# Kernel tuning notes

Measured on AMD Instinct MI355X. Metric: run time of the kernel, lower is better.

The kernel has to match this reference:

```python
import jax, jax.numpy as jnp
import numpy as np

NB = 8            # num_blocks
BS = 96           # block_size = hidden_size // num_blocks
HSF = 1           # hidden_size_factor
LAM = 0.01        # sparsity_threshold (softshrink lambda)
FRAC = 1.0        # hard_thresholding_fraction
SCALE = 0.02


def setup_inputs() -> dict:
    key = jax.random.key(0)
    ks = jax.random.split(key, 9)
    B, C, H, W, D = 2, NB * BS, 32, 32, 32
    x = jax.random.normal(ks[0], (B, C, H, W, D), jnp.float32)
    # complex params stored as separate real/imag float arrays (torch.rand on cfloat
    # fills real and imag independently with U[0,1))
    w1r = SCALE * jax.random.uniform(ks[1], (NB, BS, BS * HSF), jnp.float32)
    w1i = SCALE * jax.random.uniform(ks[2], (NB, BS, BS * HSF), jnp.float32)
    w2r = SCALE * jax.random.uniform(ks[3], (NB, BS, BS * HSF), jnp.float32)
    w2i = SCALE * jax.random.uniform(ks[4], (NB, BS, BS * HSF), jnp.float32)
    b1r = SCALE * jax.random.uniform(ks[5], (NB, BS * HSF), jnp.float32)
    b1i = SCALE * jax.random.uniform(ks[6], (NB, BS * HSF), jnp.float32)
    b2r = SCALE * jax.random.uniform(ks[7], (NB, BS), jnp.float32)
    b2i = SCALE * jax.random.uniform(ks[8], (NB, BS), jnp.float32)
    return {"x": x, "w1r": w1r, "w1i": w1i, "w2r": w2r, "w2i": w2i,
            "b1r": b1r, "b1i": b1i, "b2r": b2r, "b2i": b2i}


def _softshrink(v, lam):
    return jnp.sign(v) * jnp.maximum(jnp.abs(v) - lam, 0.0)


def _gelu_c(z):
    # torch GELU applied to view_as_real => separately on real and imag parts
    return jax.nn.gelu(jnp.real(z), approximate=False) + 1j * jax.nn.gelu(jnp.imag(z), approximate=False)


def reference(x, w1r, w1i, w2r, w2i, b1r, b1i, b2r, b2i):
    bias = x
    B, C, H, W, D = x.shape
    w1 = w1r + 1j * w1i
    w2 = w2r + 1j * w2i
    b1 = b1r + 1j * b1i
    b2 = b2r + 1j * b2i

    xf = jnp.fft.rfftn(x.astype(jnp.float32), axes=(-3, -2, -1), norm='ortho')
    Dr = xf.shape[-1]                      # D//2 + 1
    xf = xf.reshape(B, NB, BS, H, W, Dr)

    total_modes = H * W * D // 2 + 1
    kept = min(int(total_modes * FRAC), Dr)  # original slices only the last freq axis
    xk = xf[..., :kept]                      # (B, nb, bs, H, W, kept)

    # block-diagonal complex GEMM 1 + bias, then GELU on real/imag parts
    h1 = jnp.einsum('bnihwd,nio->bnohwd', xk, w1) + b1[None, :, :, None, None, None]
    h1 = _gelu_c(h1)
    # block-diagonal complex GEMM 2 + bias
    h2 = jnp.einsum('bnihwd,nio->bnohwd', h1, w2) + b2[None, :, :, None, None, None]

    # scatter back into full spectrum (zeros beyond kept modes)
    if kept < Dr:
        h2 = jnp.pad(h2, ((0, 0), (0, 0), (0, 0), (0, 0), (0, 0), (0, Dr - kept)))

    # softshrink on real/imag parts
    z = _softshrink(jnp.real(h2), LAM) + 1j * _softshrink(jnp.imag(h2), LAM)
    z = z.reshape(B, C, H, W, Dr)
    out = jnp.fft.irfftn(z, s=(H, W, D), axes=(-3, -2, -1), norm='ortho')
    return out.astype(x.dtype) + bias
```

## Files before the change

kernel.cpp:

```cpp
#include <hip/hip_runtime.h>
#include <math.h>


#define CH    768
#define DR    17
#define PLANE 544
#define NVOL  49152
#define CSTRIDE 17408
#define NTOT  26738688
#define ORTHO 0.0055242717280199026f
#define TWOPI_32 0.19634954084936207f

typedef __bf16 bf16x8 __attribute__((ext_vector_type(8)));
typedef __bf16 bf16x2 __attribute__((ext_vector_type(2)));
typedef float  f32x4  __attribute__((ext_vector_type(4)));

#define MFMA __builtin_amdgcn_mfma_f32_16x16x32_bf16

__device__ __forceinline__ float gelu_f(float v) {
    return 0.5f * v * (1.0f + erff(v * 0.7071067811865475f));
}
__device__ __forceinline__ float sshrink(float v) {
    float a = fabsf(v) - 0.01f;
    return a > 0.f ? copysignf(a, v) : 0.f;
}
__device__ __forceinline__ bf16x8 ld8(const __bf16* p) { return *(const bf16x8*)p; }
__device__ __forceinline__ void split2(float v, __bf16* h, __bf16* l) {
    __bf16 hh = (__bf16)v;
    *h = hh;
    *l = (__bf16)(v - (float)hh);
}

__device__ __align__(16) __bf16 gEf[4][1024];
__device__ __align__(16) __bf16 gEb[4][1024];
__device__ __align__(16) __bf16 gC [4][1024];

__global__ void k0_tables() {
    int idx = blockIdx.x * 256 + threadIdx.x;
    if (idx >= 1024) return;
    int c = idx & 31;
    int r = idx >> 5;
    float ang = TWOPI_32 * (float)((r * c) & 31);
    float s, co; sincosf(ang, &s, &co);
    __bf16 h, l;
    split2(co, &h, &l);  gEf[0][idx] = h; gEf[1][idx] = l;
                         gEb[0][idx] = h; gEb[1][idx] = l;
    split2(-s, &h, &l);  gEf[2][idx] = h; gEf[3][idx] = l;
    split2(s, &h, &l);   gEb[2][idx] = h; gEb[3][idx] = l;
    float cf = (c == 0 || c == 16) ? 1.f : (c < DR ? 2.f : 0.f);
    split2(cf * co, &h, &l); gC[0][idx] = h; gC[1][idx] = l;
    split2(-cf * s, &h, &l); gC[2][idx] = h; gC[3][idx] = l;
}

__device__ __align__(16) __bf16 gW1r[73728], gW1i[73728], gW2r[73728], gW2i[73728];

__global__ void k0w(const float* __restrict__ w1r, const float* __restrict__ w1i,
                    const float* __restrict__ w2r, const float* __restrict__ w2i) {
    int idx = blockIdx.x * 256 + threadIdx.x;
    if (idx >= 73728) return;
    int i = idx % 96, no = idx / 96;
    int o = no % 96, n = no / 96;
    int src = n * 9216 + i * 96 + o;
    gW1r[idx] = (__bf16)w1r[src];
    gW1i[idx] = (__bf16)w1i[src];
    gW2r[idx] = (__bf16)w2r[src];
    gW2i[idx] = (__bf16)w2i[src];
}

__global__ __launch_bounds__(256) void k1_fwd_dw(const float* __restrict__ x,
                                                 bf16x2* __restrict__ A) {
    __shared__ __align__(16) __bf16 sArh[2][32][40], sArl[2][32][40], sAih[2][32][40], sAil[2][32][40];
    const int t = threadIdx.x;
    const int wave = t >> 6, lane = t & 63, row = lane & 15, quad = lane >> 4;
    const int m0 = (wave >> 1) * 16, n0 = (wave & 1) * 16;
    const size_t pb = (size_t)blockIdx.x * 2048;

    bf16x8 xh[2], xl[2];
    #pragma unroll
    for (int pl = 0; pl < 2; pl++) {
        const float* xp = x + pb + pl * 1024 + (size_t)(m0 + row) * 32 + quad * 8;
        f32x4 x0 = *(const f32x4*)xp;
        f32x4 x1 = *(const f32x4*)(xp + 4);
        #pragma unroll
        for (int j = 0; j < 4; j++) { __bf16 h = (__bf16)x0[j]; xh[pl][j] = h; xl[pl][j] = (__bf16)(x0[j] - (float)h); }
        #pragma unroll
        for (int j = 0; j < 4; j++) { __bf16 h = (__bf16)x1[j]; xh[pl][4+j] = h; xl[pl][4+j] = (__bf16)(x1[j] - (float)h); }
    }

    {
        const int ed = (n0 + row) * 32 + quad * 8;
        bf16x8 erh = *(const bf16x8*)&gEf[0][ed];
        bf16x8 erl = *(const bf16x8*)&gEf[1][ed];
        bf16x8 eih = *(const bf16x8*)&gEf[2][ed];
        bf16x8 eil = *(const bf16x8*)&gEf[3][ed];
        #pragma unroll
        for (int pl = 0; pl < 2; pl++) {
            f32x4 ar = {0.f,0.f,0.f,0.f}, ai = {0.f,0.f,0.f,0.f};
            ar = MFMA(xh[pl], erh, ar, 0,0,0); ar = MFMA(xh[pl], erl, ar, 0,0,0); ar = MFMA(xl[pl], erh, ar, 0,0,0);
            ai = MFMA(xh[pl], eih, ai, 0,0,0); ai = MFMA(xh[pl], eil, ai, 0,0,0); ai = MFMA(xl[pl], eih, ai, 0,0,0);
            #pragma unroll
            for (int r4 = 0; r4 < 4; r4++) {
                int w = m0 + quad * 4 + r4, kd = n0 + row;
                split2(ar[r4], &sArh[pl][kd][w], &sArl[pl][kd][w]);
                split2(ai[r4], &sAih[pl][kd][w], &sAil[pl][kd][w]);
            }
        }
    }
    __syncthreads();
    {
        const int ew = (m0 + row) * 32 + quad * 8;
        bf16x8 frh = *(const bf16x8*)&gEf[0][ew];
        bf16x8 frl = *(const bf16x8*)&gEf[1][ew];
        bf16x8 fih = *(const bf16x8*)&gEf[2][ew];
        bf16x8 fil = *(const bf16x8*)&gEf[3][ew];
        const int kd = n0 + row;
        #pragma unroll
        for (int pl = 0; pl < 2; pl++) {
            bf16x8 arh = ld8(&sArh[pl][n0 + row][quad * 8]);
            bf16x8 arl = ld8(&sArl[pl][n0 + row][quad * 8]);
            bf16x8 aih = ld8(&sAih[pl][n0 + row][quad * 8]);
            bf16x8 ail = ld8(&sAil[pl][n0 + row][quad * 8]);
            f32x4 rp = {0.f,0.f,0.f,0.f}, rm = {0.f,0.f,0.f,0.f}, im = {0.f,0.f,0.f,0.f};
            rp = MFMA(frh, arh, rp, 0,0,0); rp = MFMA(frh, arl, rp, 0,0,0); rp = MFMA(frl, arh, rp, 0,0,0);
            rm = MFMA(fih, aih, rm, 0,0,0); rm = MFMA(fih, ail, rm, 0,0,0); rm = MFMA(fil, aih, rm, 0,0,0);
            im = MFMA(frh, aih, im, 0,0,0); im = MFMA(frh, ail, im, 0,0,0); im = MFMA(frl, aih, im, 0,0,0);
            im = MFMA(fih, arh, im, 0,0,0); im = MFMA(fih, arl, im, 0,0,0); im = MFMA(fil, arh, im, 0,0,0);
            if (kd < DR) {
                const size_t ab = ((size_t)blockIdx.x * 2 + pl) * PLANE;
                #pragma unroll
                for (int r4 = 0; r4 < 4; r4++) {
                    int kw = m0 + quad * 4 + r4;
                    bf16x2 o;
                    o.x = (__bf16)((rp[r4] - rm[r4]) * ORTHO);
                    o.y = (__bf16)(im[r4] * ORTHO);
                    A[ab + kw * DR + kd] = o;
                }
            }
        }
    }
}

template <bool INV>
__global__ __launch_bounds__(256) void k2_fft_h(bf16x2* __restrict__ A) {
    __shared__ __align__(16) __bf16 sBr[272][40], sBi[272][40];
    const int t = threadIdx.x;
    const int p0g = blockIdx.x * 272;
    const size_t cb = (size_t)blockIdx.y * CSTRIDE;
    for (int idx = t; idx < 8704; idx += 256) {
        int h = idx / 272, p = idx - h * 272;
        bf16x2 v = A[cb + (size_t)h * PLANE + p0g + p];
        sBr[p][h] = v.x;
        sBi[p][h] = v.y;
    }
    __syncthreads();
    const int wave = t >> 6, lane = t & 63, row = lane & 15, quad = lane >> 4;
    const __bf16* Er = gEf[0];
    const __bf16* Ei = INV ? gEb[2] : gEf[2];
    bf16x8 er0 = *(const bf16x8*)&Er[row * 32 + quad * 8];
    bf16x8 ei0 = *(const bf16x8*)&Ei[row * 32 + quad * 8];
    bf16x8 er1 = *(const bf16x8*)&Er[(16 + row) * 32 + quad * 8];
    bf16x8 ei1 = *(const bf16x8*)&Ei[(16 + row) * 32 + quad * 8];
    for (int j = wave; j < 34; j += 4) {
        int mt = j & 1, nt = j >> 1;
        int m0 = mt * 16, n0 = nt * 16;
        bf16x8 ar = mt ? er1 : er0;
        bf16x8 ai = mt ? ei1 : ei0;
        bf16x8 br = ld8(&sBr[n0 + row][quad * 8]);
        bf16x8 bi = ld8(&sBi[n0 + row][quad * 8]);
        f32x4 rp = {0.f,0.f,0.f,0.f}, rm = {0.f,0.f,0.f,0.f}, im = {0.f,0.f,0.f,0.f};
        rp = MFMA(ar, br, rp, 0, 0, 0);
        rm = MFMA(ai, bi, rm, 0, 0, 0);
        im = MFMA(ar, bi, im, 0, 0, 0);
        im = MFMA(ai, br, im, 0, 0, 0);
        int p = p0g + n0 + row;
        #pragma unroll
        for (int r = 0; r < 4; r++) {
            int kh = m0 + quad * 4 + r;
            size_t oidx = cb + (size_t)kh * PLANE + p;
            if (!INV) {
                bf16x2 o;
                o.x = (__bf16)(rp[r] - rm[r]);
                o.y = (__bf16)im[r];
                A[oidx] = o;
            } else {
                __bf16 rh, rl, ih, il;
                split2(rp[r] - rm[r], &rh, &rl);
                split2(im[r], &ih, &il);
                bf16x2 oh; oh.x = rh; oh.y = ih;
                bf16x2 ol; ol.x = rl; ol.y = il;
                A[oidx] = oh;
                A[NTOT + oidx] = ol;
            }
        }
    }
}

__global__ __launch_bounds__(256) void k3_mix(bf16x2* __restrict__ A,
    const float* __restrict__ b1r, const float* __restrict__ b1i,
    const float* __restrict__ b2r, const float* __restrict__ b2i) {
    __shared__ __align__(16) __bf16 sXr[64][104], sXi[64][104];
    const int t = threadIdx.x;
    const int chunk = blockIdx.x, bn = blockIdx.y;
    const int b = bn >> 3, n = bn & 7;
    const size_t base = (size_t)(b * CH + n * 96) * CSTRIDE + chunk * 64;

    for (int idx = t; idx < 6144; idx += 256) {
        int i = idx >> 6, p = idx & 63;
        bf16x2 v = A[base + (size_t)i * CSTRIDE + p];
        sXr[p][i] = v.x;
        sXi[p][i] = v.y;
    }
    __syncthreads();

    const int wave = t >> 6, lane = t & 63, row = lane & 15, quad = lane >> 4;
    const __bf16* W1r = &gW1r[n * 9216];
    const __bf16* W1i = &gW1i[n * 9216];
    const __bf16* W2r = &gW2r[n * 9216];
    const __bf16* W2i = &gW2i[n * 9216];
    float h1s[6][8];

    #pragma unroll
    for (int q = 0; q < 6; q++) {
        int job = wave * 6 + q, mt = job >> 2, nt = job & 3;
        int m0 = mt * 16, p0 = nt * 16;
        f32x4 rp = {0.f,0.f,0.f,0.f}, rm = {0.f,0.f,0.f,0.f}, im = {0.f,0.f,0.f,0.f};
        #pragma unroll
        for (int ks = 0; ks < 3; ks++) {
            int k0 = ks * 32 + quad * 8;
            bf16x8 ar = ld8(&W1r[(m0 + row) * 96 + k0]);
            bf16x8 ai = ld8(&W1i[(m0 + row) * 96 + k0]);
            bf16x8 br = ld8(&sXr[p0 + row][k0]);
            bf16x8 bi = ld8(&sXi[p0 + row][k0]);
            rp = MFMA(ar, br, rp, 0, 0, 0);
            rm = MFMA(ai, bi, rm, 0, 0, 0);
            im = MFMA(ar, bi, im, 0, 0, 0);
            im = MFMA(ai, br, im, 0, 0, 0);
        }
        #pragma unroll
        for (int r = 0; r < 4; r++) {
            int o = m0 + quad * 4 + r;
            float hr = b1r[n * 96 + o] + rp[r] - rm[r];
            float hi = b1i[n * 96 + o] + im[r];
            h1s[q][r]     = gelu_f(hr);
            h1s[q][4 + r] = gelu_f(hi);
        }
    }
    __syncthreads();

    #pragma unroll
    for (int q = 0; q < 6; q++) {
        int job = wave * 6 + q, mt = job >> 2, nt = job & 3;
        int m0 = mt * 16, p0 = nt * 16;
        int p = p0 + row;
        #pragma unroll
        for (int r = 0; r < 4; r++) {
            int o = m0 + quad * 4 + r;
            sXr[p][o] = (__bf16)h1s[q][r];
            sXi[p][o] = (__bf16)h1s[q][4 + r];
        }
    }
    __syncthreads();

    #pragma unroll
    for (int q = 0; q < 6; q++) {
        int job = wave * 6 + q, mt = job >> 2, nt = job & 3;
        int m0 = mt * 16, p0 = nt * 16;
        f32x4 rp = {0.f,0.f,0.f,0.f}, rm = {0.f,0.f,0.f,0.f}, im = {0.f,0.f,0.f,0.f};
        #pragma unroll
        for (int ks = 0; ks < 3; ks++) {
            int k0 = ks * 32 + quad * 8;
            bf16x8 ar = ld8(&W2r[(m0 + row) * 96 + k0]);
            bf16x8 ai = ld8(&W2i[(m0 + row) * 96 + k0]);
            bf16x8 br = ld8(&sXr[p0 + row][k0]);
            bf16x8 bi = ld8(&sXi[p0 + row][k0]);
            rp = MFMA(ar, br, rp, 0, 0, 0);
            rm = MFMA(ai, bi, rm, 0, 0, 0);
            im = MFMA(ar, bi, im, 0, 0, 0);
            im = MFMA(ai, br, im, 0, 0, 0);
        }
        int p = p0 + row;
        #pragma unroll
        for (int r = 0; r < 4; r++) {
            int o = m0 + quad * 4 + r;
            bf16x2 oV;
            oV.x = (__bf16)sshrink(b2r[n * 96 + o] + rp[r] - rm[r]);
            oV.y = (__bf16)sshrink(b2i[n * 96 + o] + im[r]);
            A[base + (size_t)o * CSTRIDE + p] = oV;
        }
    }
}

__global__ __launch_bounds__(256) void k5_inv_wd(const bf16x2* __restrict__ A,
                                                 const float* __restrict__ x,
                                                 float* __restrict__ out) {
    __shared__ __align__(16) __bf16 sZrh[32][40], sZrl[32][40], sZih[32][40], sZil[32][40];
    const int t = threadIdx.x;
    const int wave = t >> 6, lane = t & 63, row = lane & 15, quad = lane >> 4;
    const int m0 = (wave >> 1) * 16, n0 = (wave & 1) * 16;
    const size_t ab = (size_t)blockIdx.x * PLANE;
    const size_t pb = (size_t)blockIdx.x * 1024;
    const int d = n0 + row;

    float xres[4];
    #pragma unroll
    for (int r4 = 0; r4 < 4; r4++)
        xres[r4] = x[pb + (size_t)(m0 + quad * 4 + r4) * 32 + d];

    for (int idx = t; idx < PLANE; idx += 256) {
        int kw = idx / DR, kd = idx - kw * DR;
        bf16x2 h = A[ab + idx];
        bf16x2 l = A[NTOT + ab + idx];
        sZrh[kd][kw] = h.x; sZrl[kd][kw] = l.x;
        sZih[kd][kw] = h.y; sZil[kd][kw] = l.y;
    }
    for (int idx = t; idx < 480; idx += 256) {
        int kd = DR + (idx >> 5), kw = idx & 31;
        sZrh[kd][kw] = (__bf16)0.f; sZrl[kd][kw] = (__bf16)0.f;
        sZih[kd][kw] = (__bf16)0.f; sZil[kd][kw] = (__bf16)0.f;
    }
    __syncthreads();

    const int e1 = (m0 + row) * 32 + quad * 8;
    bf16x8 erh = *(const bf16x8*)&gEb[0][e1];
    bf16x8 erl = *(const bf16x8*)&gEb[1][e1];
    bf16x8 eih = *(const bf16x8*)&gEb[2][e1];
    bf16x8 eil = *(const bf16x8*)&gEb[3][e1];
    bf16x8 zrh = ld8(&sZrh[n0 + row][quad * 8]);
    bf16x8 zrl = ld8(&sZrl[n0 + row][quad * 8]);
    bf16x8 zih = ld8(&sZih[n0 + row][quad * 8]);
    bf16x8 zil = ld8(&sZil[n0 + row][quad * 8]);
    f32x4 rp = {0.f,0.f,0.f,0.f}, rm = {0.f,0.f,0.f,0.f}, im = {0.f,0.f,0.f,0.f};
    rp = MFMA(erh, zrh, rp, 0,0,0); rp = MFMA(erh, zrl, rp, 0,0,0); rp = MFMA(erl, zrh, rp, 0,0,0);
    rm = MFMA(eih, zih, rm, 0,0,0); rm = MFMA(eih, zil, rm, 0,0,0); rm = MFMA(eil, zih, rm, 0,0,0);
    im = MFMA(erh, zih, im, 0,0,0); im = MFMA(erh, zil, im, 0,0,0); im = MFMA(erl, zih, im, 0,0,0);
    im = MFMA(eih, zrh, im, 0,0,0); im = MFMA(eih, zrl, im, 0,0,0); im = MFMA(eil, zrh, im, 0,0,0);
    __syncthreads();
    #pragma unroll
    for (int r4 = 0; r4 < 4; r4++) {
        int w = m0 + quad * 4 + r4, kd = n0 + row;
        split2(rp[r4] - rm[r4], &sZrh[w][kd], &sZrl[w][kd]);
        split2(im[r4],          &sZih[w][kd], &sZil[w][kd]);
    }
    __syncthreads();

    const int c2 = d * 32 + quad * 8;
    bf16x8 crh = *(const bf16x8*)&gC[0][c2];
    bf16x8 crl = *(const bf16x8*)&gC[1][c2];
    bf16x8 cih = *(const bf16x8*)&gC[2][c2];
    bf16x8 cil = *(const bf16x8*)&gC[3][c2];
    bf16x8 grh = ld8(&sZrh[m0 + row][quad * 8]);
    bf16x8 grl = ld8(&sZrl[m0 + row][quad * 8]);
    bf16x8 gih = ld8(&sZih[m0 + row][quad * 8]);
    bf16x8 gil = ld8(&sZil[m0 + row][quad * 8]);
    f32x4 acc = {0.f,0.f,0.f,0.f};
    acc = MFMA(grh, crh, acc, 0,0,0); acc = MFMA(grh, crl, acc, 0,0,0); acc = MFMA(grl, crh, acc, 0,0,0);
    acc = MFMA(gih, cih, acc, 0,0,0); acc = MFMA(gih, cil, acc, 0,0,0); acc = MFMA(gil, cih, acc, 0,0,0);
    #pragma unroll
    for (int r4 = 0; r4 < 4; r4++) {
        int w = m0 + quad * 4 + r4;
        out[pb + (size_t)w * 32 + d] = acc[r4] * ORTHO + xres[r4];
    }
}

extern "C" void kernel_launch(void* const* d_in, const int* in_sizes, int n_in,
                              void* d_out, int out_size, void* d_ws, size_t ws_size,
                              hipStream_t stream) {
    const float* x   = (const float*)d_in[0];
    const float* w1r = (const float*)d_in[1];
    const float* w1i = (const float*)d_in[2];
    const float* w2r = (const float*)d_in[3];
    const float* w2i = (const float*)d_in[4];
    const float* b1r = (const float*)d_in[5];
    const float* b1i = (const float*)d_in[6];
    const float* b2r = (const float*)d_in[7];
    const float* b2i = (const float*)d_in[8];
    float* out = (float*)d_out;
    bf16x2* A = (bf16x2*)d_ws;

    k0_tables<<<4, 256, 0, stream>>>();
    k0w<<<288, 256, 0, stream>>>(w1r, w1i, w2r, w2i);
    k1_fwd_dw<<<NVOL / 2, 256, 0, stream>>>(x, A);
    k2_fft_h<false><<<dim3(2, 1536), 256, 0, stream>>>(A);
    k3_mix<<<dim3(272, 16), 256, 0, stream>>>(A, b1r, b1i, b2r, b2i);
    k2_fft_h<true><<<dim3(2, 1536), 256, 0, stream>>>(A);
    k5_inv_wd<<<NVOL, 256, 0, stream>>>(A, x, out);
}
```

Measured before the change: 847.6 us.

## Process more planes per block and stage mixing weights in shared memory

The forward D/W transform kernel now handles four planes per block instead of two, and the inverse W/D kernel handles two planes per block instead of one. This amortizes the per-block twiddle-table loads and launch overhead over more work. The block-diagonal mixing kernel now copies each block's W1 and then W2 weight slices into shared memory before the MFMA loops, instead of reading them from global memory in every inner iteration. The cost is more shared memory and registers per block, which may reduce occupancy, and fewer blocks in the grid.

```diff
diff --git a/kernel.cpp b/kernel.cpp
--- a/kernel.cpp
+++ b/kernel.cpp
@@ -69,15 +69,15 @@
 
 __global__ __launch_bounds__(256) void k1_fwd_dw(const float* __restrict__ x,
                                                  bf16x2* __restrict__ A) {
-    __shared__ __align__(16) __bf16 sArh[2][32][40], sArl[2][32][40], sAih[2][32][40], sAil[2][32][40];
+    __shared__ __align__(16) __bf16 sArh[4][32][40], sArl[4][32][40], sAih[4][32][40], sAil[4][32][40];
     const int t = threadIdx.x;
     const int wave = t >> 6, lane = t & 63, row = lane & 15, quad = lane >> 4;
     const int m0 = (wave >> 1) * 16, n0 = (wave & 1) * 16;
-    const size_t pb = (size_t)blockIdx.x * 2048;
-
-    bf16x8 xh[2], xl[2];
-    #pragma unroll
-    for (int pl = 0; pl < 2; pl++) {
+    const size_t pb = (size_t)blockIdx.x * 4096;
+
+    bf16x8 xh[4], xl[4];
+    #pragma unroll
+    for (int pl = 0; pl < 4; pl++) {
         const float* xp = x + pb + pl * 1024 + (size_t)(m0 + row) * 32 + quad * 8;
         f32x4 x0 = *(const f32x4*)xp;
         f32x4 x1 = *(const f32x4*)(xp + 4);
@@ -94,7 +94,7 @@
         bf16x8 eih = *(const bf16x8*)&gEf[2][ed];
         bf16x8 eil = *(const bf16x8*)&gEf[3][ed];
         #pragma unroll
-        for (int pl = 0; pl < 2; pl++) {
+        for (int pl = 0; pl < 4; pl++) {
             f32x4 ar = {0.f,0.f,0.f,0.f}, ai = {0.f,0.f,0.f,0.f};
             ar = MFMA(xh[pl], erh, ar, 0,0,0); ar = MFMA(xh[pl], erl, ar, 0,0,0); ar = MFMA(xl[pl], erh, ar, 0,0,0);
             ai = MFMA(xh[pl], eih, ai, 0,0,0); ai = MFMA(xh[pl], eil, ai, 0,0,0); ai = MFMA(xl[pl], eih, ai, 0,0,0);
@@ -115,7 +115,7 @@
         bf16x8 fil = *(const bf16x8*)&gEf[3][ew];
         const int kd = n0 + row;
         #pragma unroll
-        for (int pl = 0; pl < 2; pl++) {
+        for (int pl = 0; pl < 4; pl++) {
             bf16x8 arh = ld8(&sArh[pl][n0 + row][quad * 8]);
             bf16x8 arl = ld8(&sArl[pl][n0 + row][quad * 8]);
             bf16x8 aih = ld8(&sAih[pl][n0 + row][quad * 8]);
@@ -126,7 +126,7 @@
             im = MFMA(frh, aih, im, 0,0,0); im = MFMA(frh, ail, im, 0,0,0); im = MFMA(frl, aih, im, 0,0,0);
             im = MFMA(fih, arh, im, 0,0,0); im = MFMA(fih, arl, im, 0,0,0); im = MFMA(fil, arh, im, 0,0,0);
             if (kd < DR) {
-                const size_t ab = ((size_t)blockIdx.x * 2 + pl) * PLANE;
+                const size_t ab = ((size_t)blockIdx.x * 4 + pl) * PLANE;
                 #pragma unroll
                 for (int r4 = 0; r4 < 4; r4++) {
                     int kw = m0 + quad * 4 + r4;
@@ -198,12 +198,18 @@
 __global__ __launch_bounds__(256) void k3_mix(bf16x2* __restrict__ A,
     const float* __restrict__ b1r, const float* __restrict__ b1i,
     const float* __restrict__ b2r, const float* __restrict__ b2i) {
+    __shared__ __align__(16) __bf16 sWr[96][104], sWi[96][104];
     __shared__ __align__(16) __bf16 sXr[64][104], sXi[64][104];
     const int t = threadIdx.x;
     const int chunk = blockIdx.x, bn = blockIdx.y;
     const int b = bn >> 3, n = bn & 7;
     const size_t base = (size_t)(b * CH + n * 96) * CSTRIDE + chunk * 64;
 
+    for (int j = t; j < 1152; j += 256) {
+        int rw = j / 12, off = j - rw * 12;
+        *(bf16x8*)&sWr[rw][off * 8] = *(const bf16x8*)&gW1r[n * 9216 + j * 8];
+        *(bf16x8*)&sWi[rw][off * 8] = *(const bf16x8*)&gW1i[n * 9216 + j * 8];
+    }
     for (int idx = t; idx < 6144; idx += 256) {
         int i = idx >> 6, p = idx & 63;
         bf16x2 v = A[base + (size_t)i * CSTRIDE + p];
@@ -213,10 +219,6 @@
     __syncthreads();
 
     const int wave = t >> 6, lane = t & 63, row = lane & 15, quad = lane >> 4;
-    const __bf16* W1r = &gW1r[n * 9216];
-    const __bf16* W1i = &gW1i[n * 9216];
-    const __bf16* W2r = &gW2r[n * 9216];
-    const __bf16* W2i = &gW2i[n * 9216];
     float h1s[6][8];
 
     #pragma unroll
@@ -227,8 +229,8 @@
         #pragma unroll
         for (int ks = 0; ks < 3; ks++) {
             int k0 = ks * 32 + quad * 8;
-            bf16x8 ar = ld8(&W1r[(m0 + row) * 96 + k0]);
-            bf16x8 ai = ld8(&W1i[(m0 + row) * 96 + k0]);
+            bf16x8 ar = ld8(&sWr[m0 + row][k0]);
+            bf16x8 ai = ld8(&sWi[m0 + row][k0]);
             bf16x8 br = ld8(&sXr[p0 + row][k0]);
             bf16x8 bi = ld8(&sXi[p0 + row][k0]);
             rp = MFMA(ar, br, rp, 0, 0, 0);
@@ -259,6 +261,11 @@
             sXi[p][o] = (__bf16)h1s[q][4 + r];
         }
     }
+    for (int j = t; j < 1152; j += 256) {
+        int rw = j / 12, off = j - rw * 12;
+        *(bf16x8*)&sWr[rw][off * 8] = *(const bf16x8*)&gW2r[n * 9216 + j * 8];
+        *(bf16x8*)&sWi[rw][off * 8] = *(const bf16x8*)&gW2i[n * 9216 + j * 8];
+    }
     __syncthreads();
 
     #pragma unroll
@@ -269,8 +276,8 @@
         #pragma unroll
         for (int ks = 0; ks < 3; ks++) {
             int k0 = ks * 32 + quad * 8;
-            bf16x8 ar = ld8(&W2r[(m0 + row) * 96 + k0]);
-            bf16x8 ai = ld8(&W2i[(m0 + row) * 96 + k0]);
+            bf16x8 ar = ld8(&sWr[m0 + row][k0]);
+            bf16x8 ai = ld8(&sWi[m0 + row][k0]);
             bf16x8 br = ld8(&sXr[p0 + row][k0]);
             bf16x8 bi = ld8(&sXi[p0 + row][k0]);
             rp = MFMA(ar, br, rp, 0, 0, 0);
@@ -293,30 +300,34 @@
 __global__ __launch_bounds__(256) void k5_inv_wd(const bf16x2* __restrict__ A,
                                                  const float* __restrict__ x,
                                                  float* __restrict__ out) {
-    __shared__ __align__(16) __bf16 sZrh[32][40], sZrl[32][40], sZih[32][40], sZil[32][40];
+    __shared__ __align__(16) __bf16 sZrh[2][32][40], sZrl[2][32][40], sZih[2][32][40], sZil[2][32][40];
     const int t = threadIdx.x;
     const int wave = t >> 6, lane = t & 63, row = lane & 15, quad = lane >> 4;
     const int m0 = (wave >> 1) * 16, n0 = (wave & 1) * 16;
-    const size_t ab = (size_t)blockIdx.x * PLANE;
-    const size_t pb = (size_t)blockIdx.x * 1024;
+    const size_t ab = (size_t)blockIdx.x * (2 * PLANE);
+    const size_t pb = (size_t)blockIdx.x * 2048;
     const int d = n0 + row;
 
-    float xres[4];
-    #pragma unroll
-    for (int r4 = 0; r4 < 4; r4++)
-        xres[r4] = x[pb + (size_t)(m0 + quad * 4 + r4) * 32 + d];
-
-    for (int idx = t; idx < PLANE; idx += 256) {
-        int kw = idx / DR, kd = idx - kw * DR;
+    float xres[2][4];
+    #pragma unroll
+    for (int pl = 0; pl < 2; pl++)
+        #pragma unroll
+        for (int r4 = 0; r4 < 4; r4++)
+            xres[pl][r4] = x[pb + pl * 1024 + (size_t)(m0 + quad * 4 + r4) * 32 + d];
+
+    for (int idx = t; idx < 2 * PLANE; idx += 256) {
+        int pl = idx / PLANE, li = idx - pl * PLANE;
+        int kw = li / DR, kd = li - kw * DR;
         bf16x2 h = A[ab + idx];
         bf16x2 l = A[NTOT + ab + idx];
-        sZrh[kd][kw] = h.x; sZrl[kd][kw] = l.x;
-        sZih[kd][kw] = h.y; sZil[kd][kw] = l.y;
-    }
-    for (int idx = t; idx < 480; idx += 256) {
-        int kd = DR + (idx >> 5), kw = idx & 31;
-        sZrh[kd][kw] = (__bf16)0.f; sZrl[kd][kw] = (__bf16)0.f;
-        sZih[kd][kw] = (__bf16)0.f; sZil[kd][kw] = (__bf16)0.f;
+        sZrh[pl][kd][kw] = h.x; sZrl[pl][kd][kw] = l.x;
+        sZih[pl][kd][kw] = h.y; sZil[pl][kd][kw] = l.y;
+    }
+    for (int idx = t; idx < 960; idx += 256) {
+        int pl = idx / 480, r = idx - pl * 480;
+        int kd = DR + (r >> 5), kw = r & 31;
+        sZrh[pl][kd][kw] = (__bf16)0.f; sZrl[pl][kd][kw] = (__bf16)0.f;
+        sZih[pl][kd][kw] = (__bf16)0.f; sZil[pl][kd][kw] = (__bf16)0.f;
     }
     __syncthreads();
 
@@ -325,21 +336,30 @@
     bf16x8 erl = *(const bf16x8*)&gEb[1][e1];
     bf16x8 eih = *(const bf16x8*)&gEb[2][e1];
     bf16x8 eil = *(const bf16x8*)&gEb[3][e1];
-    bf16x8 zrh = ld8(&sZrh[n0 + row][quad * 8]);
-    bf16x8 zrl = ld8(&sZrl[n0 + row][quad * 8]);
-    bf16x8 zih = ld8(&sZih[n0 + row][quad * 8]);
-    bf16x8 zil = ld8(&sZil[n0 + row][quad * 8]);
-    f32x4 rp = {0.f,0.f,0.f,0.f}, rm = {0.f,0.f,0.f,0.f}, im = {0.f,0.f,0.f,0.f};
-    rp = MFMA(erh, zrh, rp, 0,0,0); rp = MFMA(erh, zrl, rp, 0,0,0); rp = MFMA(erl, zrh, rp, 0,0,0);
-    rm = MFMA(eih, zih, rm, 0,0,0); rm = MFMA(eih, zil, rm, 0,0,0); rm = MFMA(eil, zih, rm, 0,0,0);
-    im = MFMA(erh, zih, im, 0,0,0); im = MFMA(erh, zil, im, 0,0,0); im = MFMA(erl, zih, im, 0,0,0);
-    im = MFMA(eih, zrh, im, 0,0,0); im = MFMA(eih, zrl, im, 0,0,0); im = MFMA(eil, zrh, im, 0,0,0);
-    __syncthreads();
-    #pragma unroll
-    for (int r4 = 0; r4 < 4; r4++) {
-        int w = m0 + quad * 4 + r4, kd = n0 + row;
-        split2(rp[r4] - rm[r4], &sZrh[w][kd], &sZrl[w][kd]);
-        split2(im[r4],          &sZih[w][kd], &sZil[w][kd]);
+    f32x4 s1r[2], s1i[2];
+    #pragma unroll
+    for (int pl = 0; pl < 2; pl++) {
+        bf16x8 zrh = ld8(&sZrh[pl][n0 + row][quad * 8]);
+        bf16x8 zrl = ld8(&sZrl[pl][n0 + row][quad * 8]);
+        bf16x8 zih = ld8(&sZih[pl][n0 + row][quad * 8]);
+        bf16x8 zil = ld8(&sZil[pl][n0 + row][quad * 8]);
+        f32x4 rp = {0.f,0.f,0.f,0.f}, rm = {0.f,0.f,0.f,0.f}, im = {0.f,0.f,0.f,0.f};
+        rp = MFMA(erh, zrh, rp, 0,0,0); rp = MFMA(erh, zrl, rp, 0,0,0); rp = MFMA(erl, zrh, rp, 0,0,0);
+        rm = MFMA(eih, zih, rm, 0,0,0); rm = MFMA(eih, zil, rm, 0,0,0); rm = MFMA(eil, zih, rm, 0,0,0);
+        im = MFMA(erh, zih, im, 0,0,0); im = MFMA(erh, zil, im, 0,0,0); im = MFMA(erl, zih, im, 0,0,0);
+        im = MFMA(eih, zrh, im, 0,0,0); im = MFMA(eih, zrl, im, 0,0,0); im = MFMA(eil, zrh, im, 0,0,0);
+        s1r[pl] = rp - rm;
+        s1i[pl] = im;
+    }
+    __syncthreads();
+    #pragma unroll
+    for (int pl = 0; pl < 2; pl++) {
+        #pragma unroll
+        for (int r4 = 0; r4 < 4; r4++) {
+            int w = m0 + quad * 4 + r4, kd = n0 + row;
+            split2(s1r[pl][r4], &sZrh[pl][w][kd], &sZrl[pl][w][kd]);
+            split2(s1i[pl][r4], &sZih[pl][w][kd], &sZil[pl][w][kd]);
+        }
     }
     __syncthreads();
 
@@ -348,17 +368,20 @@
     bf16x8 crl = *(const bf16x8*)&gC[1][c2];
     bf16x8 cih = *(const bf16x8*)&gC[2][c2];
     bf16x8 cil = *(const bf16x8*)&gC[3][c2];
-    bf16x8 grh = ld8(&sZrh[m0 + row][quad * 8]);
-    bf16x8 grl = ld8(&sZrl[m0 + row][quad * 8]);
-    bf16x8 gih = ld8(&sZih[m0 + row][quad * 8]);
-    bf16x8 gil = ld8(&sZil[m0 + row][quad * 8]);
-    f32x4 acc = {0.f,0.f,0.f,0.f};
-    acc = MFMA(grh, crh, acc, 0,0,0); acc = MFMA(grh, crl, acc, 0,0,0); acc = MFMA(grl, crh, acc, 0,0,0);
-    acc = MFMA(gih, cih, acc, 0,0,0); acc = MFMA(gih, cil, acc, 0,0,0); acc = MFMA(gil, cih, acc, 0,0,0);
-    #pragma unroll
-    for (int r4 = 0; r4 < 4; r4++) {
-        int w = m0 + quad * 4 + r4;
-        out[pb + (size_t)w * 32 + d] = acc[r4] * ORTHO + xres[r4];
+    #pragma unroll
+    for (int pl = 0; pl < 2; pl++) {
+        bf16x8 grh = ld8(&sZrh[pl][m0 + row][quad * 8]);
+        bf16x8 grl = ld8(&sZrl[pl][m0 + row][quad * 8]);
+        bf16x8 gih = ld8(&sZih[pl][m0 + row][quad * 8]);
+        bf16x8 gil = ld8(&sZil[pl][m0 + row][quad * 8]);
+        f32x4 acc = {0.f,0.f,0.f,0.f};
+        acc = MFMA(grh, crh, acc, 0,0,0); acc = MFMA(grh, crl, acc, 0,0,0); acc = MFMA(grl, crh, acc, 0,0,0);
+        acc = MFMA(gih, cih, acc, 0,0,0); acc = MFMA(gih, cil, acc, 0,0,0); acc = MFMA(gil, cih, acc, 0,0,0);
+        #pragma unroll
+        for (int r4 = 0; r4 < 4; r4++) {
+            int w = m0 + quad * 4 + r4;
+            out[pb + pl * 1024 + (size_t)w * 32 + d] = acc[r4] * ORTHO + xres[pl][r4];
+        }
     }
 }
 
@@ -379,9 +402,9 @@
 
     k0_tables<<<4, 256, 0, stream>>>();
     k0w<<<288, 256, 0, stream>>>(w1r, w1i, w2r, w2i);
-    k1_fwd_dw<<<NVOL / 2, 256, 0, stream>>>(x, A);
+    k1_fwd_dw<<<NVOL / 4, 256, 0, stream>>>(x, A);
     k2_fft_h<false><<<dim3(2, 1536), 256, 0, stream>>>(A);
     k3_mix<<<dim3(272, 16), 256, 0, stream>>>(A, b1r, b1i, b2r, b2i);
     k2_fft_h<true><<<dim3(2, 1536), 256, 0, stream>>>(A);
-    k5_inv_wd<<<NVOL, 256, 0, stream>>>(A, x, out);
-}
+    k5_inv_wd<<<NVOL / 2, 256, 0, stream>>>(A, x, out);
+}
```

After: 808.4 us. 1.05x faster.
